# Optimization experiments

Hardware: AMD Instinct MI355X
Metric: run time of the kernel (lower is better)

Reference implementation:

```python
import jax, jax.numpy as jnp
import numpy as np
from itertools import combinations

B = 512
N_FEATURES = 64
BINS = 64
N_EMBED = 32
N_HIDDEN = 128
N_OUTPUT = 1
GAMMA = 1.0
TOTAL = N_FEATURES * BINS  # sum(feature_sizes) = 4096


def setup_inputs() -> dict:
    key = jax.random.key(0)
    ks = jax.random.split(key, 20)
    P = N_FEATURES * (N_FEATURES - 1) // 2  # 2016
    mains = jax.random.randint(ks[0], (B, N_FEATURES), 0, BINS, dtype=jnp.int32)
    pairs = jax.random.randint(ks[1], (B, P, 2), 0, BINS, dtype=jnp.int32)
    emb = jax.random.normal(ks[2], (TOTAL, N_EMBED), dtype=jnp.float32) * 0.05
    s = 0.05
    mw0 = jax.random.normal(ks[3], (N_FEATURES, N_EMBED, N_HIDDEN), jnp.float32) * s
    mw1 = jax.random.normal(ks[4], (N_FEATURES, N_HIDDEN, N_HIDDEN), jnp.float32) * s
    mw2 = jax.random.normal(ks[5], (N_FEATURES, N_HIDDEN, N_OUTPUT), jnp.float32) * s
    mb0 = jax.random.normal(ks[6], (N_FEATURES, N_HIDDEN), jnp.float32) * s
    mb1 = jax.random.normal(ks[7], (N_FEATURES, N_HIDDEN), jnp.float32) * s
    mb2 = jax.random.normal(ks[8], (N_FEATURES, N_OUTPUT), jnp.float32) * s
    z_main = jax.random.uniform(ks[9], (N_FEATURES,), jnp.float32, -GAMMA / 100, GAMMA / 100)
    pw0 = jax.random.normal(ks[10], (P, 2 * N_EMBED, N_HIDDEN), jnp.float32) * s
    pw1 = jax.random.normal(ks[11], (P, N_HIDDEN, N_HIDDEN), jnp.float32) * s
    pw2 = jax.random.normal(ks[12], (P, N_HIDDEN, N_OUTPUT), jnp.float32) * s
    pb0 = jax.random.normal(ks[13], (P, N_HIDDEN), jnp.float32) * s
    pb1 = jax.random.normal(ks[14], (P, N_HIDDEN), jnp.float32) * s
    pb2 = jax.random.normal(ks[15], (P, N_OUTPUT), jnp.float32) * s
    z_pairs = jax.random.uniform(ks[16], (P,), jnp.float32, -GAMMA / 100, GAMMA / 100)
    pairs_list = jnp.asarray(np.array(list(combinations(range(N_FEATURES), 2)), dtype=np.int32))
    feature_offsets = (jnp.arange(N_FEATURES, dtype=jnp.int32) * BINS)
    return dict(mains=mains, pairs=pairs, emb=emb,
                mw0=mw0, mw1=mw1, mw2=mw2, mb0=mb0, mb1=mb1, mb2=mb2, z_main=z_main,
                pw0=pw0, pw1=pw1, pw2=pw2, pb0=pb0, pb1=pb1, pb2=pb2, z_pairs=z_pairs,
                pairs_list=pairs_list, feature_offsets=feature_offsets)


def _smooth_z(z):
    g = GAMMA
    smooth = (-2.0 / g ** 3) * z ** 3 + (3.0 / (2.0 * g)) * z + 0.5
    return jnp.where(z <= -g / 2, 0.0, jnp.where(z >= g / 2, 1.0, smooth))


def _grouped_mlp(h, ws, bs):
    # h: [B, G, d_in]; ws[i]: [G, d_in_i, d_out_i]; relu on all but last layer
    n = len(ws)
    for i, (w, b) in enumerate(zip(ws, bs)):
        h = jnp.einsum('bgk,gkl->bgl', h, w) + b[None]
        if i < n - 1:
            h = jax.nn.relu(h)
    return h


def reference(mains, pairs, emb, mw0, mw1, mw2, mb0, mb1, mb2, z_main,
              pw0, pw1, pw2, pb0, pb1, pb2, z_pairs, pairs_list, feature_offsets):
    # main effects: per-feature embedding gather + per-feature MLP
    main_idx = mains + feature_offsets[None, :]             # [B, F]
    h = emb[main_idx]                                        # [B, F, E]
    h = _grouped_mlp(h, [mw0, mw1, mw2], [mb0, mb1, mb2])    # [B, F, O]
    zm = _smooth_z(z_main)                                   # [F]
    out_main = jnp.einsum('bfo,f->bo', h, zm)                # [B, O]
    # pair effects: gather both feature embeddings, concat, per-pair MLP
    pair_off = feature_offsets[pairs_list]                   # [P, 2]
    pair_idx = pairs + pair_off[None]                        # [B, P, 2]
    e = emb[pair_idx]                                        # [B, P, 2, E]
    Bp, P = e.shape[0], e.shape[1]
    e = e.reshape(Bp, P, 2 * e.shape[-1])                    # [B, P, 2E]
    hp = _grouped_mlp(e, [pw0, pw1, pw2], [pb0, pb1, pb2])   # [B, P, O]
    zp = _smooth_z(z_pairs)                                  # [P]
    out_pairs = jnp.einsum('bpo,p->bo', hp, zp)              # [B, O]
    return out_main + out_pairs
```

## Files before the change

kernel.cpp:

```cpp
#include <hip/hip_runtime.h>


typedef _Float16 f16x8 __attribute__((ext_vector_type(8)));
typedef float f32x4 __attribute__((ext_vector_type(4)));

constexpr int Bsz = 512;
constexpr int NF  = 64;
constexpr int NE  = 32;
constexpr int NH  = 128;
constexpr int NP  = 2016;
constexpr int NG  = NP + NF;
constexpr int BT  = 64;
constexpr int NSEG = 8, GSEG = NG / NSEG;

constexpr size_t WS_S2 = (size_t)NG * Bsz;
constexpr size_t WS_PT = WS_S2 + (size_t)NSEG * Bsz;

__device__ __forceinline__ float smoothz(float z) {
  float s = fmaf(-2.0f * z * z, z, fmaf(1.5f, z, 0.5f));
  if (z <= -0.5f) s = 0.0f;
  if (z >=  0.5f) s = 1.0f;
  return s;
}

__device__ __forceinline__ void put_sw(_Float16* base, int ldk, int row, int k,
                                       float v) {
  base[row * ldk + (((k >> 3) ^ (row & 7)) * 8) + (k & 7)] = (_Float16)v;
}

__global__ void transpose_pairs_kernel(const int* __restrict__ pairs,
                                       int* __restrict__ pt) {
  __shared__ int tile[32][33];
  const int bt = blockIdx.x;
  const int qt = blockIdx.y;
  const int t  = threadIdx.x;
  const int tq = t & 7, tb = t >> 3;
  const int brow  = bt * 32 + tb;
  const int qbase = qt * 32 + tq * 4;
#pragma unroll
  for (int j = 0; j < 4; ++j)
    tile[tb][tq * 4 + j] = pairs[brow * (2 * NP) + qbase + j];
  __syncthreads();
  const int ob = t & 7, oq = t >> 3;
  const int qrow = qt * 32 + oq;
#pragma unroll
  for (int j = 0; j < 4; ++j)
    pt[(size_t)qrow * Bsz + bt * 32 + ob * 4 + j] = tile[ob * 4 + j][oq];
}

__global__ __launch_bounds__(256, 2) void fused_groups_kernel(
    const int* __restrict__ mains, const int* __restrict__ pt,
    const float* __restrict__ emb,
    const float* __restrict__ mw0, const float* __restrict__ mw1,
    const float* __restrict__ mw2, const float* __restrict__ mb0,
    const float* __restrict__ mb1, const float* __restrict__ mb2,
    const float* __restrict__ z_main,
    const float* __restrict__ pw0, const float* __restrict__ pw1,
    const float* __restrict__ pw2, const float* __restrict__ pb0,
    const float* __restrict__ pb1, const float* __restrict__ pb2,
    const float* __restrict__ z_pairs,
    const int* __restrict__ pairs_list, const int* __restrict__ foff,
    float* __restrict__ ws) {
  __shared__ _Float16 sW0[NH * 64];
  __shared__ _Float16 sW1[NH * NH];
  __shared__ _Float16 sA[BT * 64];
  __shared__ _Float16 sH[BT * NH];
  __shared__ float    sRed[4 * BT];

  const int t    = threadIdx.x;
  const int wave = t >> 6;
  const int lane = t & 63;
  const int l    = lane & 15;
  const int qd   = lane >> 4;
  const int wnb  = wave * 32;
  const int g    = blockIdx.x;
  const bool is_pair = (g < NP);

  const float *W0, *W1, *w2p, *bv0, *bv1;
  float b2s, z;
  int kc0, off0 = 0, off1 = 0, fid = 0;
  if (is_pair) {
    W0  = pw0 + (size_t)g * (2 * NE * NH);
    W1  = pw1 + (size_t)g * (NH * NH);
    w2p = pw2 + (size_t)g * NH;
    bv0 = pb0 + (size_t)g * NH;
    bv1 = pb1 + (size_t)g * NH;
    b2s = pb2[g];
    z   = smoothz(z_pairs[g]);
    kc0 = 2;
    off0 = foff[pairs_list[2 * g + 0]];
    off1 = foff[pairs_list[2 * g + 1]];
  } else {
    fid = g - NP;
    W0  = mw0 + (size_t)fid * (NE * NH);
    W1  = mw1 + (size_t)fid * (NH * NH);
    w2p = mw2 + (size_t)fid * NH;
    bv0 = mb0 + (size_t)fid * NH;
    bv1 = mb1 + (size_t)fid * NH;
    b2s = mb2[fid];
    z   = smoothz(z_main[fid]);
    kc0 = 1;
    off0 = foff[fid];
  }

  float b0v[2], b1v[2], wv2[2];
#pragma unroll
  for (int nc = 0; nc < 2; ++nc) {
    const int col = wnb + nc * 16 + l;
    b0v[nc] = bv0[col];
    b1v[nc] = bv1[col];
    wv2[nc] = w2p[col];
  }

#pragma unroll 2
  for (int i = 0; i < kc0 * 4; ++i) {
    const int f = (t + i * 256) * 4;
    const float4 v = *(const float4*)(W0 + f);
    const int k = f >> 7, c = f & 127;
    put_sw(sW0, 64, c + 0, k, v.x);
    put_sw(sW0, 64, c + 1, k, v.y);
    put_sw(sW0, 64, c + 2, k, v.z);
    put_sw(sW0, 64, c + 3, k, v.w);
  }
#pragma unroll 4
  for (int i = 0; i < 16; ++i) {
    const int f = (t + i * 256) * 4;
    const float4 v = *(const float4*)(W1 + f);
    const int k = f >> 7, c = f & 127;
    put_sw(sW1, NH, c + 0, k, v.x);
    put_sw(sW1, NH, c + 1, k, v.y);
    put_sw(sW1, NH, c + 2, k, v.z);
    put_sw(sW1, NH, c + 3, k, v.w);
  }

  const int col0 = wnb + l, col1 = wnb + 16 + l;
  const int cs0 = (col0 & 7), cs1 = (col1 & 7);

  for (int tile = 0; tile < Bsz / BT; ++tile) {
    const int bbase = tile * BT;
    __syncthreads();

    {
      const int row = t & 63;
      const int q   = t >> 6;
      const int b   = bbase + row;
      if (is_pair) {
        const int which = q >> 1;
        const int bin = pt[(size_t)(2 * g + which) * Bsz + b];
        const int idx = bin + (which ? off1 : off0);
        const float* er = emb + (size_t)idx * NE + (q & 1) * 16;
        const float4 e0 = ((const float4*)er)[0];
        const float4 e1 = ((const float4*)er)[1];
        const float4 e2 = ((const float4*)er)[2];
        const float4 e3 = ((const float4*)er)[3];
        f16x8 h0, h1;
        h0[0] = (_Float16)e0.x; h0[1] = (_Float16)e0.y;
        h0[2] = (_Float16)e0.z; h0[3] = (_Float16)e0.w;
        h0[4] = (_Float16)e1.x; h0[5] = (_Float16)e1.y;
        h0[6] = (_Float16)e1.z; h0[7] = (_Float16)e1.w;
        h1[0] = (_Float16)e2.x; h1[1] = (_Float16)e2.y;
        h1[2] = (_Float16)e2.z; h1[3] = (_Float16)e2.w;
        h1[4] = (_Float16)e3.x; h1[5] = (_Float16)e3.y;
        h1[6] = (_Float16)e3.z; h1[7] = (_Float16)e3.w;
        const int blk0 = (2 * q)     ^ (row & 7);
        const int blk1 = (2 * q + 1) ^ (row & 7);
        *(f16x8*)&sA[row * 64 + blk0 * 8] = h0;
        *(f16x8*)&sA[row * 64 + blk1 * 8] = h1;
      } else {
        const int bin = mains[b * NF + fid];
        const int idx = bin + off0;
        const float* er = emb + (size_t)idx * NE + q * 8;
        const float4 e0 = ((const float4*)er)[0];
        const float4 e1 = ((const float4*)er)[1];
        f16x8 h0;
        h0[0] = (_Float16)e0.x; h0[1] = (_Float16)e0.y;
        h0[2] = (_Float16)e0.z; h0[3] = (_Float16)e0.w;
        h0[4] = (_Float16)e1.x; h0[5] = (_Float16)e1.y;
        h0[6] = (_Float16)e1.z; h0[7] = (_Float16)e1.w;
        const int blk = q ^ (row & 7);
        *(f16x8*)&sA[row * 64 + blk * 8] = h0;
      }
    }
    __syncthreads();

    f32x4 acc0[4][2];
#pragma unroll
    for (int m = 0; m < 4; ++m)
#pragma unroll
      for (int nc = 0; nc < 2; ++nc)
        acc0[m][nc] = (f32x4){b0v[nc], b0v[nc], b0v[nc], b0v[nc]};

    for (int kc = 0; kc < kc0; ++kc) {
      const int kb = kc * 4 + qd;
      const f16x8 bf0 = *(const f16x8*)&sW0[col0 * 64 + ((kb ^ cs0) * 8)];
      const f16x8 bf1 = *(const f16x8*)&sW0[col1 * 64 + ((kb ^ cs1) * 8)];
#pragma unroll
      for (int m = 0; m < 4; ++m) {
        const int brow = m * 16 + l;
        const f16x8 af = *(const f16x8*)&sA[brow * 64 + ((kb ^ (brow & 7)) * 8)];
        acc0[m][0] = __builtin_amdgcn_mfma_f32_16x16x32_f16(af, bf0, acc0[m][0], 0, 0, 0);
        acc0[m][1] = __builtin_amdgcn_mfma_f32_16x16x32_f16(af, bf1, acc0[m][1], 0, 0, 0);
      }
    }

#pragma unroll
    for (int m = 0; m < 4; ++m)
#pragma unroll
      for (int nc = 0; nc < 2; ++nc)
#pragma unroll
        for (int r = 0; r < 4; ++r) {
          const float v = fmaxf(acc0[m][nc][r], 0.0f);
          const int row = m * 16 + qd * 4 + r;
          const int col = wnb + nc * 16 + l;
          sH[row * NH + (((col >> 3) ^ (row & 7)) * 8) + (col & 7)] =
              (_Float16)v;
        }
    __syncthreads();

    f32x4 acc1[4][2];
#pragma unroll
    for (int m = 0; m < 4; ++m)
#pragma unroll
      for (int nc = 0; nc < 2; ++nc)
        acc1[m][nc] = (f32x4){b1v[nc], b1v[nc], b1v[nc], b1v[nc]};

#pragma unroll
    for (int kc = 0; kc < 4; ++kc) {
      const int kb = kc * 4 + qd;
      const f16x8 bf0 = *(const f16x8*)&sW1[col0 * NH + ((kb ^ cs0) * 8)];
      const f16x8 bf1 = *(const f16x8*)&sW1[col1 * NH + ((kb ^ cs1) * 8)];
#pragma unroll
      for (int m = 0; m < 4; ++m) {
        const int brow = m * 16 + l;
        const f16x8 af = *(const f16x8*)&sH[brow * NH + ((kb ^ (brow & 7)) * 8)];
        acc1[m][0] = __builtin_amdgcn_mfma_f32_16x16x32_f16(af, bf0, acc1[m][0], 0, 0, 0);
        acc1[m][1] = __builtin_amdgcn_mfma_f32_16x16x32_f16(af, bf1, acc1[m][1], 0, 0, 0);
      }
    }

    float v16[16];
#pragma unroll
    for (int m = 0; m < 4; ++m)
#pragma unroll
      for (int r = 0; r < 4; ++r)
        v16[m * 4 + r] = fmaf(fmaxf(acc1[m][0][r], 0.0f), wv2[0],
                              fmaxf(acc1[m][1][r], 0.0f) * wv2[1]);

    const int lb0 = l & 1, lb1 = (l >> 1) & 1, lb2 = (l >> 2) & 1,
              lb3 = (l >> 3) & 1;
    float v8[8];
#pragma unroll
    for (int i = 0; i < 8; ++i) {
      const float mine   = lb0 ? v16[2 * i + 1] : v16[2 * i];
      const float theirs = lb0 ? v16[2 * i]     : v16[2 * i + 1];
      v8[i] = mine + __shfl_xor(theirs, 1, 64);
    }
    float v4[4];
#pragma unroll
    for (int i = 0; i < 4; ++i) {
      const float mine   = lb1 ? v8[2 * i + 1] : v8[2 * i];
      const float theirs = lb1 ? v8[2 * i]     : v8[2 * i + 1];
      v4[i] = mine + __shfl_xor(theirs, 2, 64);
    }
    float v2[2];
#pragma unroll
    for (int i = 0; i < 2; ++i) {
      const float mine   = lb2 ? v4[2 * i + 1] : v4[2 * i];
      const float theirs = lb2 ? v4[2 * i]     : v4[2 * i + 1];
      v2[i] = mine + __shfl_xor(theirs, 4, 64);
    }
    const float mine1   = lb3 ? v2[1] : v2[0];
    const float theirs1 = lb3 ? v2[0] : v2[1];
    const float v1 = mine1 + __shfl_xor(theirs1, 8, 64);

    const int row_local = (l >> 2) * 16 + qd * 4 + (l & 3);
    sRed[wave * BT + row_local] = v1;
    __syncthreads();
    if (t < BT) {
      const float s =
          sRed[t] + sRed[BT + t] + sRed[2 * BT + t] + sRed[3 * BT + t];
      ws[(size_t)g * Bsz + bbase + t] = (s + b2s) * z;
    }
  }
}

__global__ void reduce1_kernel(const float* __restrict__ part,
                               float* __restrict__ s2) {
  const int b   = blockIdx.x * 256 + threadIdx.x;
  const int seg = blockIdx.y;
  float s = 0.0f;
#pragma unroll 8
  for (int g = seg * GSEG; g < (seg + 1) * GSEG; ++g)
    s += part[(size_t)g * Bsz + b];
  s2[seg * Bsz + b] = s;
}

__global__ void reduce2_kernel(const float* __restrict__ s2,
                               float* __restrict__ out) {
  const int b = blockIdx.x * 256 + threadIdx.x;
  float s = 0.0f;
#pragma unroll
  for (int k = 0; k < NSEG; ++k) s += s2[k * Bsz + b];
  out[b] = s;
}

extern "C" void kernel_launch(void* const* d_in, const int* in_sizes, int n_in,
                              void* d_out, int out_size, void* d_ws,
                              size_t ws_size, hipStream_t stream) {
  const int*   mains      = (const int*)d_in[0];
  const int*   pairs      = (const int*)d_in[1];
  const float* emb        = (const float*)d_in[2];
  const float* mw0        = (const float*)d_in[3];
  const float* mw1        = (const float*)d_in[4];
  const float* mw2        = (const float*)d_in[5];
  const float* mb0        = (const float*)d_in[6];
  const float* mb1        = (const float*)d_in[7];
  const float* mb2        = (const float*)d_in[8];
  const float* z_main     = (const float*)d_in[9];
  const float* pw0        = (const float*)d_in[10];
  const float* pw1        = (const float*)d_in[11];
  const float* pw2        = (const float*)d_in[12];
  const float* pb0        = (const float*)d_in[13];
  const float* pb1        = (const float*)d_in[14];
  const float* pb2        = (const float*)d_in[15];
  const float* z_pairs    = (const float*)d_in[16];
  const int*   pairs_list = (const int*)d_in[17];
  const int*   foff       = (const int*)d_in[18];
  float* ws   = (float*)d_ws;
  float* out  = (float*)d_out;
  float* part = ws;
  float* s2   = ws + WS_S2;
  int*   pt   = (int*)(ws + WS_PT);

  transpose_pairs_kernel<<<dim3(16, 126), 256, 0, stream>>>(pairs, pt);
  fused_groups_kernel<<<NG, 256, 0, stream>>>(
      mains, pt, emb, mw0, mw1, mw2, mb0, mb1, mb2, z_main, pw0, pw1, pw2,
      pb0, pb1, pb2, z_pairs, pairs_list, foff, part);
  reduce1_kernel<<<dim3(2, NSEG), 256, 0, stream>>>(part, s2);
  reduce2_kernel<<<2, 256, 0, stream>>>(s2, out);
}
```

Before: 395.2 us.

## Hold per-group MLP weights in register fragments instead of LDS

Weight matrices W0 and W1 are no longer staged into shared memory. Each wave now loads its own column fragments straight from global memory into registers as f16 MFMA operands. The product is transposed so weights act as the A operand and activations as B, which lets the output reduction use a cross-quad shuffle instead of a butterfly. LDS use drops and launch bounds rise to 3 blocks per CU to raise occupancy. The risks are strided, uncoalesced global weight loads and high register pressure, and one tile-loop barrier has also been removed.

```diff
diff --git a/kernel.cpp b/kernel.cpp
--- a/kernel.cpp
+++ b/kernel.cpp
@@ -2,6 +2,7 @@
 
 
 typedef _Float16 f16x8 __attribute__((ext_vector_type(8)));
+typedef _Float16 f16x4 __attribute__((ext_vector_type(4)));
 typedef float f32x4 __attribute__((ext_vector_type(4)));
 
 constexpr int Bsz = 512;
@@ -21,11 +22,6 @@
   if (z <= -0.5f) s = 0.0f;
   if (z >=  0.5f) s = 1.0f;
   return s;
-}
-
-__device__ __forceinline__ void put_sw(_Float16* base, int ldk, int row, int k,
-                                       float v) {
-  base[row * ldk + (((k >> 3) ^ (row & 7)) * 8) + (k & 7)] = (_Float16)v;
 }
 
 __global__ void transpose_pairs_kernel(const int* __restrict__ pairs,
@@ -48,7 +44,14 @@
     pt[(size_t)qrow * Bsz + bt * 32 + ob * 4 + j] = tile[ob * 4 + j][oq];
 }
 
-__global__ __launch_bounds__(256, 2) void fused_groups_kernel(
+__device__ __forceinline__ f16x8 load_col_frag(const float* __restrict__ p) {
+  f16x8 f;
+#pragma unroll
+  for (int j = 0; j < 8; ++j) f[j] = (_Float16)p[(size_t)(j * NH)];
+  return f;
+}
+
+__global__ __launch_bounds__(256, 3) void fused_groups_kernel(
     const int* __restrict__ mains, const int* __restrict__ pt,
     const float* __restrict__ emb,
     const float* __restrict__ mw0, const float* __restrict__ mw1,
@@ -61,24 +64,22 @@
     const float* __restrict__ z_pairs,
     const int* __restrict__ pairs_list, const int* __restrict__ foff,
     float* __restrict__ ws) {
-  __shared__ _Float16 sW0[NH * 64];
-  __shared__ _Float16 sW1[NH * NH];
   __shared__ _Float16 sA[BT * 64];
   __shared__ _Float16 sH[BT * NH];
-  __shared__ float    sRed[4 * BT];
+  __shared__ __align__(16) float sBias[3 * NH];
+  __shared__ float sRed[4 * BT];
 
   const int t    = threadIdx.x;
   const int wave = t >> 6;
   const int lane = t & 63;
   const int l    = lane & 15;
   const int qd   = lane >> 4;
-  const int wnb  = wave * 32;
   const int g    = blockIdx.x;
   const bool is_pair = (g < NP);
 
   const float *W0, *W1, *w2p, *bv0, *bv1;
   float b2s, z;
-  int kc0, off0 = 0, off1 = 0, fid = 0;
+  int off0 = 0, off1 = 0, fid = 0;
   if (is_pair) {
     W0  = pw0 + (size_t)g * (2 * NE * NH);
     W1  = pw1 + (size_t)g * (NH * NH);
@@ -87,7 +88,6 @@
     bv1 = pb1 + (size_t)g * NH;
     b2s = pb2[g];
     z   = smoothz(z_pairs[g]);
-    kc0 = 2;
     off0 = foff[pairs_list[2 * g + 0]];
     off1 = foff[pairs_list[2 * g + 1]];
   } else {
@@ -99,46 +99,36 @@
     bv1 = mb1 + (size_t)fid * NH;
     b2s = mb2[fid];
     z   = smoothz(z_main[fid]);
-    kc0 = 1;
     off0 = foff[fid];
   }
 
-  float b0v[2], b1v[2], wv2[2];
-#pragma unroll
-  for (int nc = 0; nc < 2; ++nc) {
-    const int col = wnb + nc * 16 + l;
-    b0v[nc] = bv0[col];
-    b1v[nc] = bv1[col];
-    wv2[nc] = w2p[col];
+  if (t < 96) {
+    const int which = t >> 5;
+    const int i = (t & 31) * 4;
+    const float* src = which == 0 ? bv0 : (which == 1 ? bv1 : w2p);
+    *(float4*)&sBias[which * NH + i] = *(const float4*)(src + i);
   }
 
-#pragma unroll 2
-  for (int i = 0; i < kc0 * 4; ++i) {
-    const int f = (t + i * 256) * 4;
-    const float4 v = *(const float4*)(W0 + f);
-    const int k = f >> 7, c = f & 127;
-    put_sw(sW0, 64, c + 0, k, v.x);
-    put_sw(sW0, 64, c + 1, k, v.y);
-    put_sw(sW0, 64, c + 2, k, v.z);
-    put_sw(sW0, 64, c + 3, k, v.w);
+  const int hq = wave * 32 + l;
+  f16x8 w0f[2][2];
+  f16x8 w1f[2][4];
+#pragma unroll
+  for (int mh = 0; mh < 2; ++mh) {
+    const float* base0 = W0 + (size_t)(qd * 8) * NH + (hq + mh * 16);
+    w0f[mh][0] = load_col_frag(base0);
+    if (is_pair) w0f[mh][1] = load_col_frag(base0 + (size_t)32 * NH);
   }
-#pragma unroll 4
-  for (int i = 0; i < 16; ++i) {
-    const int f = (t + i * 256) * 4;
-    const float4 v = *(const float4*)(W1 + f);
-    const int k = f >> 7, c = f & 127;
-    put_sw(sW1, NH, c + 0, k, v.x);
-    put_sw(sW1, NH, c + 1, k, v.y);
-    put_sw(sW1, NH, c + 2, k, v.z);
-    put_sw(sW1, NH, c + 3, k, v.w);
-  }
-
-  const int col0 = wnb + l, col1 = wnb + 16 + l;
-  const int cs0 = (col0 & 7), cs1 = (col1 & 7);
+#pragma unroll
+  for (int mh = 0; mh < 2; ++mh)
+#pragma unroll
+    for (int kb = 0; kb < 4; ++kb)
+      w1f[mh][kb] =
+          load_col_frag(W1 + (size_t)(kb * 32 + qd * 8) * NH + (hq + mh * 16));
+
+  const int hq4 = wave * 32 + qd * 4;
 
   for (int tile = 0; tile < Bsz / BT; ++tile) {
     const int bbase = tile * BT;
-    __syncthreads();
 
     {
       const int row = t & 63;
@@ -183,98 +173,87 @@
     }
     __syncthreads();
 
-    f32x4 acc0[4][2];
-#pragma unroll
-    for (int m = 0; m < 4; ++m)
-#pragma unroll
-      for (int nc = 0; nc < 2; ++nc)
-        acc0[m][nc] = (f32x4){b0v[nc], b0v[nc], b0v[nc], b0v[nc]};
-
-    for (int kc = 0; kc < kc0; ++kc) {
-      const int kb = kc * 4 + qd;
-      const f16x8 bf0 = *(const f16x8*)&sW0[col0 * 64 + ((kb ^ cs0) * 8)];
-      const f16x8 bf1 = *(const f16x8*)&sW0[col1 * 64 + ((kb ^ cs1) * 8)];
-#pragma unroll
-      for (int m = 0; m < 4; ++m) {
-        const int brow = m * 16 + l;
-        const f16x8 af = *(const f16x8*)&sA[brow * 64 + ((kb ^ (brow & 7)) * 8)];
-        acc0[m][0] = __builtin_amdgcn_mfma_f32_16x16x32_f16(af, bf0, acc0[m][0], 0, 0, 0);
-        acc0[m][1] = __builtin_amdgcn_mfma_f32_16x16x32_f16(af, bf1, acc0[m][1], 0, 0, 0);
+    f32x4 acc0[2][4];
+#pragma unroll
+    for (int mh = 0; mh < 2; ++mh) {
+      const f32x4 b0q = *(const f32x4*)&sBias[hq4 + mh * 16];
+#pragma unroll
+      for (int nb = 0; nb < 4; ++nb) acc0[mh][nb] = b0q;
+    }
+#pragma unroll
+    for (int nb = 0; nb < 4; ++nb) {
+      const int b  = nb * 16 + l;
+      const int rs = b & 7;
+      const f16x8 e0 = *(const f16x8*)&sA[b * 64 + ((qd ^ rs) * 8)];
+      acc0[0][nb] = __builtin_amdgcn_mfma_f32_16x16x32_f16(w0f[0][0], e0,
+                                                           acc0[0][nb], 0, 0, 0);
+      acc0[1][nb] = __builtin_amdgcn_mfma_f32_16x16x32_f16(w0f[1][0], e0,
+                                                           acc0[1][nb], 0, 0, 0);
+      if (is_pair) {
+        const f16x8 e1 = *(const f16x8*)&sA[b * 64 + (((4 + qd) ^ rs) * 8)];
+        acc0[0][nb] = __builtin_amdgcn_mfma_f32_16x16x32_f16(w0f[0][1], e1,
+                                                             acc0[0][nb], 0, 0, 0);
+        acc0[1][nb] = __builtin_amdgcn_mfma_f32_16x16x32_f16(w0f[1][1], e1,
+                                                             acc0[1][nb], 0, 0, 0);
       }
     }
 
 #pragma unroll
-    for (int m = 0; m < 4; ++m)
-#pragma unroll
-      for (int nc = 0; nc < 2; ++nc)
-#pragma unroll
-        for (int r = 0; r < 4; ++r) {
-          const float v = fmaxf(acc0[m][nc][r], 0.0f);
-          const int row = m * 16 + qd * 4 + r;
-          const int col = wnb + nc * 16 + l;
-          sH[row * NH + (((col >> 3) ^ (row & 7)) * 8) + (col & 7)] =
-              (_Float16)v;
-        }
+    for (int mh = 0; mh < 2; ++mh) {
+      const int hb = hq4 + mh * 16;
+#pragma unroll
+      for (int nb = 0; nb < 4; ++nb) {
+        const int b = nb * 16 + l;
+        f16x4 h4;
+#pragma unroll
+        for (int r = 0; r < 4; ++r)
+          h4[r] = (_Float16)fmaxf(acc0[mh][nb][r], 0.0f);
+        const int blk = (hb >> 3) ^ (b & 7);
+        *(f16x4*)&sH[b * NH + blk * 8 + (hb & 7)] = h4;
+      }
+    }
     __syncthreads();
 
-    f32x4 acc1[4][2];
-#pragma unroll
-    for (int m = 0; m < 4; ++m)
-#pragma unroll
-      for (int nc = 0; nc < 2; ++nc)
-        acc1[m][nc] = (f32x4){b1v[nc], b1v[nc], b1v[nc], b1v[nc]};
-
-#pragma unroll
-    for (int kc = 0; kc < 4; ++kc) {
-      const int kb = kc * 4 + qd;
-      const f16x8 bf0 = *(const f16x8*)&sW1[col0 * NH + ((kb ^ cs0) * 8)];
-      const f16x8 bf1 = *(const f16x8*)&sW1[col1 * NH + ((kb ^ cs1) * 8)];
-#pragma unroll
-      for (int m = 0; m < 4; ++m) {
-        const int brow = m * 16 + l;
-        const f16x8 af = *(const f16x8*)&sH[brow * NH + ((kb ^ (brow & 7)) * 8)];
-        acc1[m][0] = __builtin_amdgcn_mfma_f32_16x16x32_f16(af, bf0, acc1[m][0], 0, 0, 0);
-        acc1[m][1] = __builtin_amdgcn_mfma_f32_16x16x32_f16(af, bf1, acc1[m][1], 0, 0, 0);
+    f32x4 acc1[2][4];
+#pragma unroll
+    for (int mh = 0; mh < 2; ++mh) {
+      const f32x4 b1q = *(const f32x4*)&sBias[NH + hq4 + mh * 16];
+#pragma unroll
+      for (int nb = 0; nb < 4; ++nb) acc1[mh][nb] = b1q;
+    }
+#pragma unroll
+    for (int kb = 0; kb < 4; ++kb) {
+#pragma unroll
+      for (int nb = 0; nb < 4; ++nb) {
+        const int b = nb * 16 + l;
+        const f16x8 hf =
+            *(const f16x8*)&sH[b * NH + (((kb * 4 + qd) ^ (b & 7)) * 8)];
+        acc1[0][nb] = __builtin_amdgcn_mfma_f32_16x16x32_f16(w1f[0][kb], hf,
+                                                             acc1[0][nb], 0, 0, 0);
+        acc1[1][nb] = __builtin_amdgcn_mfma_f32_16x16x32_f16(w1f[1][kb], hf,
+                                                             acc1[1][nb], 0, 0, 0);
       }
     }
 
-    float v16[16];
-#pragma unroll
-    for (int m = 0; m < 4; ++m)
-#pragma unroll
-      for (int r = 0; r < 4; ++r)
-        v16[m * 4 + r] = fmaf(fmaxf(acc1[m][0][r], 0.0f), wv2[0],
-                              fmaxf(acc1[m][1][r], 0.0f) * wv2[1]);
-
-    const int lb0 = l & 1, lb1 = (l >> 1) & 1, lb2 = (l >> 2) & 1,
-              lb3 = (l >> 3) & 1;
-    float v8[8];
-#pragma unroll
-    for (int i = 0; i < 8; ++i) {
-      const float mine   = lb0 ? v16[2 * i + 1] : v16[2 * i];
-      const float theirs = lb0 ? v16[2 * i]     : v16[2 * i + 1];
-      v8[i] = mine + __shfl_xor(theirs, 1, 64);
-    }
-    float v4[4];
-#pragma unroll
-    for (int i = 0; i < 4; ++i) {
-      const float mine   = lb1 ? v8[2 * i + 1] : v8[2 * i];
-      const float theirs = lb1 ? v8[2 * i]     : v8[2 * i + 1];
-      v4[i] = mine + __shfl_xor(theirs, 2, 64);
-    }
-    float v2[2];
-#pragma unroll
-    for (int i = 0; i < 2; ++i) {
-      const float mine   = lb2 ? v4[2 * i + 1] : v4[2 * i];
-      const float theirs = lb2 ? v4[2 * i]     : v4[2 * i + 1];
-      v2[i] = mine + __shfl_xor(theirs, 4, 64);
-    }
-    const float mine1   = lb3 ? v2[1] : v2[0];
-    const float theirs1 = lb3 ? v2[0] : v2[1];
-    const float v1 = mine1 + __shfl_xor(theirs1, 8, 64);
-
-    const int row_local = (l >> 2) * 16 + qd * 4 + (l & 3);
-    sRed[wave * BT + row_local] = v1;
+    float yp[4] = {0.0f, 0.0f, 0.0f, 0.0f};
+#pragma unroll
+    for (int mh = 0; mh < 2; ++mh) {
+      const f32x4 w2q = *(const f32x4*)&sBias[2 * NH + hq4 + mh * 16];
+#pragma unroll
+      for (int nb = 0; nb < 4; ++nb)
+#pragma unroll
+        for (int r = 0; r < 4; ++r)
+          yp[nb] = fmaf(fmaxf(acc1[mh][nb][r], 0.0f), w2q[r], yp[nb]);
+    }
+#pragma unroll
+    for (int nb = 0; nb < 4; ++nb) {
+      yp[nb] += __shfl_xor(yp[nb], 16, 64);
+      yp[nb] += __shfl_xor(yp[nb], 32, 64);
+    }
+    if (qd == 0) {
+#pragma unroll
+      for (int nb = 0; nb < 4; ++nb) sRed[wave * BT + nb * 16 + l] = yp[nb];
+    }
     __syncthreads();
     if (t < BT) {
       const float s =
```

Result: faster. 339.5 us (-14.1%).
